# Kernel optimization log

Measured on AMD Instinct MI355X. Metric: run time of the kernel, lower is better.

## Reference

```python
import jax, jax.numpy as jnp
import numpy as np

BN_EPS = 1e-3  # O-CNN default bn_eps


def setup_inputs() -> dict:
    key = jax.random.key(0)
    k1, k2, k3 = jax.random.split(key, 3)
    N, Cin, Cout, K = 100000, 32, 32, 27  # nodes, channels, 3x3x3 taps
    data_in = jax.random.normal(k1, (1, Cin, N, 1), dtype=jnp.float32)
    neigh = jax.random.randint(k2, (N, K), 0, N, dtype=jnp.int32)
    weight = jax.random.normal(k3, (K, Cin, Cout), dtype=jnp.float32) * 0.05
    gamma = jnp.ones((Cout,), dtype=jnp.float32)
    beta = jnp.zeros((Cout,), dtype=jnp.float32)
    return {"data_in": data_in, "neigh": neigh, "weight": weight,
            "gamma": gamma, "beta": beta}


def reference(data_in, neigh, weight, gamma, beta):
    # data_in: [1, Cin, N, 1] -> x: [N, Cin]
    x = data_in[0, :, :, 0].T
    # Octree conv: gather 27 neighbor features per node, then small matmul.
    col = x[neigh]                                   # [N, 27, Cin] (irregular gather)
    y = jnp.einsum('nkc,kcd->nd', col, weight)       # [N, Cout]
    # BatchNorm2d in training mode: stats over the N (spatial) axis.
    mean = jnp.mean(y, axis=0)
    var = jnp.mean(jnp.square(y - mean), axis=0)     # biased variance, as BN uses
    yn = (y - mean) * jax.lax.rsqrt(var + BN_EPS) * gamma + beta
    # back to O-CNN layout [1, Cout, N, 1]
    return yn.T[None, :, :, None]
```

## Files before the change

### kernel.cpp

```cpp
#include <hip/hip_runtime.h>

#define KK 27

typedef short bf16x8 __attribute__((ext_vector_type(8)));
typedef float f32x4  __attribute__((ext_vector_type(4)));

__device__ inline unsigned short f2bf(float f) {
    unsigned u = __float_as_uint(f);
    unsigned r = u + 0x7fffu + ((u >> 16) & 1u);
    return (unsigned short)(r >> 16);
}

__global__ __launch_bounds__(256) void prep_k(const float* __restrict__ in,
                                              const float* __restrict__ w,
                                              unsigned short* __restrict__ xTb,
                                              unsigned short* __restrict__ wTb,
                                              float* __restrict__ tot,
                                              int N, int nxblk) {
    __shared__ float tile[32][33];
    const int b = blockIdx.x;
    if (b < nxblk) {
        int n0 = b * 32;
        int tx = threadIdx.x & 31;
        int ty = threadIdx.x >> 5;
#pragma unroll
        for (int c = ty; c < 32; c += 8) {
            int n = n0 + tx;
            tile[c][tx] = (n < N) ? in[(long)c * N + n] : 0.f;
        }
        __syncthreads();
#pragma unroll
        for (int nn = ty; nn < 32; nn += 8) {
            int n = n0 + nn;
            if (n < N) xTb[(long)n * 32 + tx] = f2bf(tile[tx][nn]);
        }
        if (b == 0 && threadIdx.x < 32) xTb[(long)N * 32 + threadIdx.x] = 0;
    } else {
        int k = b - nxblk;
        for (int i = threadIdx.x; i < 1024; i += 256) {
            int cin = i >> 5, cout = i & 31;
            wTb[k * 1024 + cout * 32 + cin] = f2bf(w[k * 1024 + cin * 32 + cout]);
        }
        if (k == 0) {
            for (int i = threadIdx.x; i < 32 * 64; i += 256) tot[i] = 0.f;
        }
    }
}

__global__ __launch_bounds__(256, 4) void conv_k(const unsigned short* __restrict__ xTb,
                                                 const int* __restrict__ neigh,
                                                 const unsigned short* __restrict__ wTb,
                                                 float* __restrict__ y,
                                                 float* __restrict__ tot,
                                                 int N) {
    __shared__ float ct[4][32][33];

    const int tid  = threadIdx.x;
    const int L    = tid & 63;
    const int w    = tid >> 6;
    const int r16  = L & 15;
    const int quad = L >> 4;
    const int base = blockIdx.x * 128 + w * 32;
    const int n0 = base + r16;
    const int n1 = base + 16 + r16;
    const bool v0 = (n0 < N), v1 = (n1 < N);
    const long nb0 = (long)(v0 ? n0 : 0) * KK;
    const long nb1 = (long)(v1 ? n1 : 0) * KK;

    f32x4 acc00 = {0.f, 0.f, 0.f, 0.f};
    f32x4 acc01 = acc00, acc10 = acc00, acc11 = acc00;

    int ia = v0 ? neigh[nb0] : N;
    int ib = v1 ? neigh[nb1] : N;
    int ja = v0 ? neigh[nb0 + 1] : N;
    int jb = v1 ? neigh[nb1 + 1] : N;

    bf16x8 a0 = *(const bf16x8*)(xTb + (long)ia * 32 + quad * 8);
    bf16x8 a1 = *(const bf16x8*)(xTb + (long)ib * 32 + quad * 8);
    bf16x8 b0 = *(const bf16x8*)(wTb + r16 * 32 + quad * 8);
    bf16x8 b1 = *(const bf16x8*)(wTb + (16 + r16) * 32 + quad * 8);

#pragma unroll 1
    for (int k = 0; k < KK; ++k) {
        bf16x8 na0, na1, pb0, pb1;
        if (k < KK - 1) {
            na0 = *(const bf16x8*)(xTb + (long)ja * 32 + quad * 8);
            na1 = *(const bf16x8*)(xTb + (long)jb * 32 + quad * 8);
            const unsigned short* wn = wTb + (k + 1) * 1024;
            pb0 = *(const bf16x8*)(wn + r16 * 32 + quad * 8);
            pb1 = *(const bf16x8*)(wn + (16 + r16) * 32 + quad * 8);
            int kk = (k + 2 < KK) ? (k + 2) : (KK - 1);
            ja = v0 ? neigh[nb0 + kk] : N;
            jb = v1 ? neigh[nb1 + kk] : N;
        }

        acc00 = __builtin_amdgcn_mfma_f32_16x16x32_bf16(a0, b0, acc00, 0, 0, 0);
        acc01 = __builtin_amdgcn_mfma_f32_16x16x32_bf16(a0, b1, acc01, 0, 0, 0);
        acc10 = __builtin_amdgcn_mfma_f32_16x16x32_bf16(a1, b0, acc10, 0, 0, 0);
        acc11 = __builtin_amdgcn_mfma_f32_16x16x32_bf16(a1, b1, acc11, 0, 0, 0);

        if (k < KK - 1) {
            a0 = na0;
            a1 = na1;
            b0 = pb0;
            b1 = pb1;
        }
    }

    float s0 = 0.f, q0 = 0.f, s1 = 0.f, q1 = 0.f;
#pragma unroll
    for (int r = 0; r < 4; ++r) {
        s0 += acc00[r] + acc10[r];
        q0 += acc00[r] * acc00[r] + acc10[r] * acc10[r];
        s1 += acc01[r] + acc11[r];
        q1 += acc01[r] * acc01[r] + acc11[r] * acc11[r];
    }
#pragma unroll
    for (int off = 16; off < 64; off <<= 1) {
        s0 += __shfl_xor(s0, off, 64);
        q0 += __shfl_xor(q0, off, 64);
        s1 += __shfl_xor(s1, off, 64);
        q1 += __shfl_xor(q1, off, 64);
    }
    const int stripe = (blockIdx.x * 4 + w) & 31;
    if (L < 16) {
        float* tb = tot + stripe * 64;
        atomicAdd(&tb[L],      s0);
        atomicAdd(&tb[L + 16], s1);
        atomicAdd(&tb[L + 32], q0);
        atomicAdd(&tb[L + 48], q1);
    }

#pragma unroll
    for (int r = 0; r < 4; ++r) {
        ct[w][quad * 4 + r][r16]           = acc00[r];
        ct[w][quad * 4 + r][16 + r16]      = acc01[r];
        ct[w][16 + quad * 4 + r][r16]      = acc10[r];
        ct[w][16 + quad * 4 + r][16 + r16] = acc11[r];
    }
    const int node = L & 31;
    const int half = L >> 5;
    const int gn = base + node;
    if (gn < N) {
#pragma unroll
        for (int i = 0; i < 16; ++i) {
            const int cout = i * 2 + half;
            y[(long)cout * N + gn] = ct[w][node][cout];
        }
    }
}

__global__ __launch_bounds__(256) void norm_k(float* __restrict__ y,
                                              const float* __restrict__ tot,
                                              const float* __restrict__ gamma,
                                              const float* __restrict__ beta, int N) {
    const int d = blockIdx.y;
    float sm = 0.f, sq = 0.f;
#pragma unroll
    for (int s = 0; s < 32; ++s) {
        sm += tot[s * 64 + d];
        sq += tot[s * 64 + 32 + d];
    }
    const float mean = sm / (float)N;
    const float var  = sq / (float)N - mean * mean;
    const float sc   = gamma[d] * rsqrtf(var + 1e-3f);
    const float sh   = beta[d] - mean * sc;

    int i = blockIdx.x * blockDim.x + threadIdx.x;
    int base = i * 4;
    if (base + 3 < N) {
        float4* p = (float4*)(y + (long)d * N + base);
        float4 v = *p;
        v.x = fmaf(v.x, sc, sh);
        v.y = fmaf(v.y, sc, sh);
        v.z = fmaf(v.z, sc, sh);
        v.w = fmaf(v.w, sc, sh);
        *p = v;
    } else if (base < N) {
        for (int t = base; t < N; ++t) y[(long)d * N + t] = fmaf(y[(long)d * N + t], sc, sh);
    }
}

extern "C" void kernel_launch(void* const* d_in, const int* in_sizes, int n_in,
                              void* d_out, int out_size, void* d_ws, size_t ws_size,
                              hipStream_t stream) {
    const float* data_in = (const float*)d_in[0];
    const int*   neigh   = (const int*)d_in[1];
    const float* weight  = (const float*)d_in[2];
    const float* gamma   = (const float*)d_in[3];
    const float* beta    = (const float*)d_in[4];
    float* out = (float*)d_out;

    const int N = in_sizes[1] / KK;
    const int nxblk   = (N + 31) / 32;
    const int nblk128 = (N + 127) / 128;

    char* ws = (char*)d_ws;
    unsigned short* xTb = (unsigned short*)ws;
    unsigned short* wTb = (unsigned short*)(ws + (size_t)(N + 1) * 64);
    float* tot = (float*)(ws + (size_t)(N + 1) * 64 + 55296);

    prep_k<<<nxblk + KK, 256, 0, stream>>>(data_in, weight, xTb, wTb, tot, N, nxblk);
    conv_k<<<nblk128, 256, 0, stream>>>(xTb, neigh, wTb, out, tot, N);
    dim3 ngrid(((N + 3) / 4 + 255) / 256, 32);
    norm_k<<<ngrid, 256, 0, stream>>>(out, tot, gamma, beta, N);
}
```

Before: 146.8 us.

## Split bf16 features into channel halves and pair taps per MFMA

Measured after the change: 153.1 us. +4.3%, slower.

```diff
diff --git a/kernel.cpp b/kernel.cpp
--- a/kernel.cpp
+++ b/kernel.cpp
@@ -1,6 +1,8 @@
 #include <hip/hip_runtime.h>
 
+
 #define KK 27
+#define PT 14
 
 typedef short bf16x8 __attribute__((ext_vector_type(8)));
 typedef float f32x4  __attribute__((ext_vector_type(4)));
@@ -13,8 +15,10 @@
 
 __global__ __launch_bounds__(256) void prep_k(const float* __restrict__ in,
                                               const float* __restrict__ w,
-                                              unsigned short* __restrict__ xTb,
-                                              unsigned short* __restrict__ wTb,
+                                              unsigned short* __restrict__ xLo,
+                                              unsigned short* __restrict__ xHi,
+                                              unsigned short* __restrict__ wP0,
+                                              unsigned short* __restrict__ wP1,
                                               float* __restrict__ tot,
                                               int N, int nxblk) {
     __shared__ float tile[32][33];
@@ -32,35 +36,53 @@
 #pragma unroll
         for (int nn = ty; nn < 32; nn += 8) {
             int n = n0 + nn;
-            if (n < N) xTb[(long)n * 32 + tx] = f2bf(tile[tx][nn]);
-        }
-        if (b == 0 && threadIdx.x < 32) xTb[(long)N * 32 + threadIdx.x] = 0;
+            if (n < N) {
+                unsigned short v = f2bf(tile[tx][nn]);
+                if (tx < 16) xLo[(long)n * 16 + tx]        = v;
+                else         xHi[(long)n * 16 + (tx - 16)] = v;
+            }
+        }
+        if (b == 0 && threadIdx.x < 32) {
+            int t = threadIdx.x;
+            if (t < 16) xLo[(long)N * 16 + t]        = 0;
+            else        xHi[(long)N * 16 + (t - 16)] = 0;
+        }
     } else {
-        int k = b - nxblk;
+        int t = b - nxblk;
         for (int i = threadIdx.x; i < 1024; i += 256) {
-            int cin = i >> 5, cout = i & 31;
-            wTb[k * 1024 + cout * 32 + cin] = f2bf(w[k * 1024 + cin * 32 + cout]);
-        }
-        if (k == 0) {
+            int cout = i >> 5, k32 = i & 31;
+            int tap = 2 * t + (k32 >> 4);
+            int c   = k32 & 15;
+            unsigned short lo = 0, hi = 0;
+            if (tap < KK) {
+                lo = f2bf(w[tap * 1024 + c * 32 + cout]);
+                hi = f2bf(w[tap * 1024 + (c + 16) * 32 + cout]);
+            }
+            wP0[t * 1024 + cout * 32 + k32] = lo;
+            wP1[t * 1024 + cout * 32 + k32] = hi;
+        }
+        if (t == 0) {
             for (int i = threadIdx.x; i < 32 * 64; i += 256) tot[i] = 0.f;
         }
     }
 }
 
-__global__ __launch_bounds__(256, 4) void conv_k(const unsigned short* __restrict__ xTb,
-                                                 const int* __restrict__ neigh,
-                                                 const unsigned short* __restrict__ wTb,
-                                                 float* __restrict__ y,
-                                                 float* __restrict__ tot,
-                                                 int N) {
-    __shared__ float ct[4][32][33];
-
-    const int tid  = threadIdx.x;
-    const int L    = tid & 63;
-    const int w    = tid >> 6;
+__global__ __launch_bounds__(64, 4) void conv_k(const unsigned short* __restrict__ xLo,
+                                                const unsigned short* __restrict__ xHi,
+                                                const int* __restrict__ neigh,
+                                                const unsigned short* __restrict__ wP0,
+                                                const unsigned short* __restrict__ wP1,
+                                                float* __restrict__ y,
+                                                float* __restrict__ tot,
+                                                int N) {
+    __shared__ float ct[32][33];
+
+    const int L    = threadIdx.x;
     const int r16  = L & 15;
     const int quad = L >> 4;
-    const int base = blockIdx.x * 128 + w * 32;
+    const int tapsel = quad >> 1;
+    const int off8   = (quad & 1) * 8;
+    const int base = blockIdx.x * 32;
     const int n0 = base + r16;
     const int n1 = base + 16 + r16;
     const bool v0 = (n0 < N), v1 = (n1 < N);
@@ -70,40 +92,51 @@
     f32x4 acc00 = {0.f, 0.f, 0.f, 0.f};
     f32x4 acc01 = acc00, acc10 = acc00, acc11 = acc00;
 
-    int ia = v0 ? neigh[nb0] : N;
-    int ib = v1 ? neigh[nb1] : N;
-    int ja = v0 ? neigh[nb0 + 1] : N;
-    int jb = v1 ? neigh[nb1 + 1] : N;
-
-    bf16x8 a0 = *(const bf16x8*)(xTb + (long)ia * 32 + quad * 8);
-    bf16x8 a1 = *(const bf16x8*)(xTb + (long)ib * 32 + quad * 8);
-    bf16x8 b0 = *(const bf16x8*)(wTb + r16 * 32 + quad * 8);
-    bf16x8 b1 = *(const bf16x8*)(wTb + (16 + r16) * 32 + quad * 8);
+    auto ldidx = [&](long nb, bool v, int kq) -> int {
+        int kc = (kq < KK) ? kq : (KK - 1);
+        int j  = __builtin_nontemporal_load(neigh + nb + kc);
+        return (v && kq < KK) ? j : N;
+    };
 
 #pragma unroll 1
-    for (int k = 0; k < KK; ++k) {
-        bf16x8 na0, na1, pb0, pb1;
-        if (k < KK - 1) {
-            na0 = *(const bf16x8*)(xTb + (long)ja * 32 + quad * 8);
-            na1 = *(const bf16x8*)(xTb + (long)jb * 32 + quad * 8);
-            const unsigned short* wn = wTb + (k + 1) * 1024;
-            pb0 = *(const bf16x8*)(wn + r16 * 32 + quad * 8);
-            pb1 = *(const bf16x8*)(wn + (16 + r16) * 32 + quad * 8);
-            int kk = (k + 2 < KK) ? (k + 2) : (KK - 1);
-            ja = v0 ? neigh[nb0 + kk] : N;
-            jb = v1 ? neigh[nb1 + kk] : N;
-        }
-
-        acc00 = __builtin_amdgcn_mfma_f32_16x16x32_bf16(a0, b0, acc00, 0, 0, 0);
-        acc01 = __builtin_amdgcn_mfma_f32_16x16x32_bf16(a0, b1, acc01, 0, 0, 0);
-        acc10 = __builtin_amdgcn_mfma_f32_16x16x32_bf16(a1, b0, acc10, 0, 0, 0);
-        acc11 = __builtin_amdgcn_mfma_f32_16x16x32_bf16(a1, b1, acc11, 0, 0, 0);
-
-        if (k < KK - 1) {
-            a0 = na0;
-            a1 = na1;
-            b0 = pb0;
-            b1 = pb1;
+    for (int ph = 0; ph < 2; ++ph) {
+        const unsigned short* __restrict__ xp = ph ? xHi : xLo;
+        const unsigned short* __restrict__ wp = ph ? wP1 : wP0;
+
+        int ia = ldidx(nb0, v0, tapsel);
+        int ib = ldidx(nb1, v1, tapsel);
+        int ja = ldidx(nb0, v0, 2 + tapsel);
+        int jb = ldidx(nb1, v1, 2 + tapsel);
+
+        bf16x8 a0 = *(const bf16x8*)(xp + (long)ia * 16 + off8);
+        bf16x8 a1 = *(const bf16x8*)(xp + (long)ib * 16 + off8);
+        bf16x8 b0 = *(const bf16x8*)(wp + r16 * 32 + quad * 8);
+        bf16x8 b1 = *(const bf16x8*)(wp + (16 + r16) * 32 + quad * 8);
+
+#pragma unroll 1
+        for (int t = 0; t < PT; ++t) {
+            bf16x8 na0, na1, pb0, pb1;
+            if (t < PT - 1) {
+                na0 = *(const bf16x8*)(xp + (long)ja * 16 + off8);
+                na1 = *(const bf16x8*)(xp + (long)jb * 16 + off8);
+                const unsigned short* wn = wp + (t + 1) * 1024;
+                pb0 = *(const bf16x8*)(wn + r16 * 32 + quad * 8);
+                pb1 = *(const bf16x8*)(wn + (16 + r16) * 32 + quad * 8);
+                ja = ldidx(nb0, v0, 2 * (t + 2) + tapsel);
+                jb = ldidx(nb1, v1, 2 * (t + 2) + tapsel);
+            }
+
+            acc00 = __builtin_amdgcn_mfma_f32_16x16x32_bf16(a0, b0, acc00, 0, 0, 0);
+            acc01 = __builtin_amdgcn_mfma_f32_16x16x32_bf16(a0, b1, acc01, 0, 0, 0);
+            acc10 = __builtin_amdgcn_mfma_f32_16x16x32_bf16(a1, b0, acc10, 0, 0, 0);
+            acc11 = __builtin_amdgcn_mfma_f32_16x16x32_bf16(a1, b1, acc11, 0, 0, 0);
+
+            if (t < PT - 1) {
+                a0 = na0;
+                a1 = na1;
+                b0 = pb0;
+                b1 = pb1;
+            }
         }
     }
 
@@ -122,7 +155,7 @@
         s1 += __shfl_xor(s1, off, 64);
         q1 += __shfl_xor(q1, off, 64);
     }
-    const int stripe = (blockIdx.x * 4 + w) & 31;
+    const int stripe = blockIdx.x & 31;
     if (L < 16) {
         float* tb = tot + stripe * 64;
         atomicAdd(&tb[L],      s0);
@@ -133,11 +166,12 @@
 
 #pragma unroll
     for (int r = 0; r < 4; ++r) {
-        ct[w][quad * 4 + r][r16]           = acc00[r];
-        ct[w][quad * 4 + r][16 + r16]      = acc01[r];
-        ct[w][16 + quad * 4 + r][r16]      = acc10[r];
-        ct[w][16 + quad * 4 + r][16 + r16] = acc11[r];
-    }
+        ct[quad * 4 + r][r16]           = acc00[r];
+        ct[quad * 4 + r][16 + r16]      = acc01[r];
+        ct[16 + quad * 4 + r][r16]      = acc10[r];
+        ct[16 + quad * 4 + r][16 + r16] = acc11[r];
+    }
+    __syncthreads();
     const int node = L & 31;
     const int half = L >> 5;
     const int gn = base + node;
@@ -145,7 +179,7 @@
 #pragma unroll
         for (int i = 0; i < 16; ++i) {
             const int cout = i * 2 + half;
-            y[(long)cout * N + gn] = ct[w][node][cout];
+            __builtin_nontemporal_store(ct[node][cout], y + (long)cout * N + gn);
         }
     }
 }
@@ -192,16 +226,19 @@
     float* out = (float*)d_out;
 
     const int N = in_sizes[1] / KK;
-    const int nxblk   = (N + 31) / 32;
-    const int nblk128 = (N + 127) / 128;
+    const int nxblk = (N + 31) / 32;
+    const int nblk  = (N + 31) / 32;
 
     char* ws = (char*)d_ws;
-    unsigned short* xTb = (unsigned short*)ws;
-    unsigned short* wTb = (unsigned short*)(ws + (size_t)(N + 1) * 64);
-    float* tot = (float*)(ws + (size_t)(N + 1) * 64 + 55296);
-
-    prep_k<<<nxblk + KK, 256, 0, stream>>>(data_in, weight, xTb, wTb, tot, N, nxblk);
-    conv_k<<<nblk128, 256, 0, stream>>>(xTb, neigh, wTb, out, tot, N);
+    size_t halfBytes = (size_t)(N + 1) * 32;
+    unsigned short* xLo = (unsigned short*)ws;
+    unsigned short* xHi = (unsigned short*)(ws + halfBytes);
+    unsigned short* wP0 = (unsigned short*)(ws + 2 * halfBytes);
+    unsigned short* wP1 = wP0 + PT * 1024;
+    float* tot = (float*)((char*)(wP1 + PT * 1024));
+
+    prep_k<<<nxblk + PT, 256, 0, stream>>>(data_in, weight, xLo, xHi, wP0, wP1, tot, N, nxblk);
+    conv_k<<<nblk, 64, 0, stream>>>(xLo, xHi, neigh, wP0, wP1, out, tot, N);
     dim3 ngrid(((N + 3) / 4 + 255) / 256, 32);
     norm_k<<<ngrid, 256, 0, stream>>>(out, tot, gamma, beta, N);
 }
```

## Split tap loop into two interleaved streams and use one-wave blocks

Applied to the files above, without the earlier changes.

Measured after the change: 135.7 us. -7.5%, faster.

```diff
diff --git a/kernel.cpp b/kernel.cpp
--- a/kernel.cpp
+++ b/kernel.cpp
@@ -47,20 +47,18 @@
     }
 }
 
-__global__ __launch_bounds__(256, 4) void conv_k(const unsigned short* __restrict__ xTb,
-                                                 const int* __restrict__ neigh,
-                                                 const unsigned short* __restrict__ wTb,
-                                                 float* __restrict__ y,
-                                                 float* __restrict__ tot,
-                                                 int N) {
-    __shared__ float ct[4][32][33];
-
-    const int tid  = threadIdx.x;
-    const int L    = tid & 63;
-    const int w    = tid >> 6;
+__global__ __launch_bounds__(64, 4) void conv_k(const unsigned short* __restrict__ xTb,
+                                                const int* __restrict__ neigh,
+                                                const unsigned short* __restrict__ wTb,
+                                                float* __restrict__ y,
+                                                float* __restrict__ tot,
+                                                int N) {
+    __shared__ float ct[32][33];
+
+    const int L    = threadIdx.x;
     const int r16  = L & 15;
     const int quad = L >> 4;
-    const int base = blockIdx.x * 128 + w * 32;
+    const int base = blockIdx.x * 32;
     const int n0 = base + r16;
     const int n1 = base + 16 + r16;
     const bool v0 = (n0 < N), v1 = (n1 < N);
@@ -70,40 +68,60 @@
     f32x4 acc00 = {0.f, 0.f, 0.f, 0.f};
     f32x4 acc01 = acc00, acc10 = acc00, acc11 = acc00;
 
-    int ia = v0 ? neigh[nb0] : N;
-    int ib = v1 ? neigh[nb1] : N;
-    int ja = v0 ? neigh[nb0 + 1] : N;
-    int jb = v1 ? neigh[nb1 + 1] : N;
-
-    bf16x8 a0 = *(const bf16x8*)(xTb + (long)ia * 32 + quad * 8);
-    bf16x8 a1 = *(const bf16x8*)(xTb + (long)ib * 32 + quad * 8);
-    bf16x8 b0 = *(const bf16x8*)(wTb + r16 * 32 + quad * 8);
-    bf16x8 b1 = *(const bf16x8*)(wTb + (16 + r16) * 32 + quad * 8);
+    int iA0 = v0 ? neigh[nb0 + 0]  : N;
+    int iA1 = v1 ? neigh[nb1 + 0]  : N;
+    int iB0 = v0 ? neigh[nb0 + 14] : N;
+    int iB1 = v1 ? neigh[nb1 + 14] : N;
+
+    bf16x8 xA0 = *(const bf16x8*)(xTb + (long)iA0 * 32 + quad * 8);
+    bf16x8 xA1 = *(const bf16x8*)(xTb + (long)iA1 * 32 + quad * 8);
+    bf16x8 xB0 = *(const bf16x8*)(xTb + (long)iB0 * 32 + quad * 8);
+    bf16x8 xB1 = *(const bf16x8*)(xTb + (long)iB1 * 32 + quad * 8);
+
+    bf16x8 wA0 = *(const bf16x8*)(wTb + r16 * 32 + quad * 8);
+    bf16x8 wA1 = *(const bf16x8*)(wTb + (16 + r16) * 32 + quad * 8);
+    bf16x8 wB0 = *(const bf16x8*)(wTb + 14 * 1024 + r16 * 32 + quad * 8);
+    bf16x8 wB1 = *(const bf16x8*)(wTb + 14 * 1024 + (16 + r16) * 32 + quad * 8);
+
+    iA0 = v0 ? neigh[nb0 + 1]  : N;
+    iA1 = v1 ? neigh[nb1 + 1]  : N;
+    iB0 = v0 ? neigh[nb0 + 15] : N;
+    iB1 = v1 ? neigh[nb1 + 15] : N;
 
 #pragma unroll 1
-    for (int k = 0; k < KK; ++k) {
-        bf16x8 na0, na1, pb0, pb1;
-        if (k < KK - 1) {
-            na0 = *(const bf16x8*)(xTb + (long)ja * 32 + quad * 8);
-            na1 = *(const bf16x8*)(xTb + (long)jb * 32 + quad * 8);
-            const unsigned short* wn = wTb + (k + 1) * 1024;
-            pb0 = *(const bf16x8*)(wn + r16 * 32 + quad * 8);
-            pb1 = *(const bf16x8*)(wn + (16 + r16) * 32 + quad * 8);
-            int kk = (k + 2 < KK) ? (k + 2) : (KK - 1);
-            ja = v0 ? neigh[nb0 + kk] : N;
-            jb = v1 ? neigh[nb1 + kk] : N;
-        }
-
-        acc00 = __builtin_amdgcn_mfma_f32_16x16x32_bf16(a0, b0, acc00, 0, 0, 0);
-        acc01 = __builtin_amdgcn_mfma_f32_16x16x32_bf16(a0, b1, acc01, 0, 0, 0);
-        acc10 = __builtin_amdgcn_mfma_f32_16x16x32_bf16(a1, b0, acc10, 0, 0, 0);
-        acc11 = __builtin_amdgcn_mfma_f32_16x16x32_bf16(a1, b1, acc11, 0, 0, 0);
-
-        if (k < KK - 1) {
-            a0 = na0;
-            a1 = na1;
-            b0 = pb0;
-            b1 = pb1;
+    for (int i = 0; i < 14; ++i) {
+        bf16x8 nxA0, nxA1, nxB0, nxB1, nwA0, nwA1, nwB0, nwB1;
+        if (i < 13) {
+            nxA0 = *(const bf16x8*)(xTb + (long)iA0 * 32 + quad * 8);
+            nxA1 = *(const bf16x8*)(xTb + (long)iA1 * 32 + quad * 8);
+            nxB0 = *(const bf16x8*)(xTb + (long)iB0 * 32 + quad * 8);
+            nxB1 = *(const bf16x8*)(xTb + (long)iB1 * 32 + quad * 8);
+            const unsigned short* wa = wTb + (i + 1) * 1024;
+            const int kb = (15 + i <= 26) ? (15 + i) : 26;
+            const unsigned short* wb = wTb + kb * 1024;
+            nwA0 = *(const bf16x8*)(wa + r16 * 32 + quad * 8);
+            nwA1 = *(const bf16x8*)(wa + (16 + r16) * 32 + quad * 8);
+            nwB0 = *(const bf16x8*)(wb + r16 * 32 + quad * 8);
+            nwB1 = *(const bf16x8*)(wb + (16 + r16) * 32 + quad * 8);
+            const int ka2 = (i + 2 <= 13) ? (i + 2) : 13;
+            const int kb2 = (16 + i <= 26) ? (16 + i) : 26;
+            iA0 = v0 ? neigh[nb0 + ka2] : N;
+            iA1 = v1 ? neigh[nb1 + ka2] : N;
+            iB0 = v0 ? neigh[nb0 + kb2] : N;
+            iB1 = v1 ? neigh[nb1 + kb2] : N;
+        }
+
+        acc00 = __builtin_amdgcn_mfma_f32_16x16x32_bf16(xA0, wA0, acc00, 0, 0, 0);
+        acc01 = __builtin_amdgcn_mfma_f32_16x16x32_bf16(xA0, wA1, acc01, 0, 0, 0);
+        acc10 = __builtin_amdgcn_mfma_f32_16x16x32_bf16(xA1, wA0, acc10, 0, 0, 0);
+        acc11 = __builtin_amdgcn_mfma_f32_16x16x32_bf16(xA1, wA1, acc11, 0, 0, 0);
+        if (i < 13) {
+            acc00 = __builtin_amdgcn_mfma_f32_16x16x32_bf16(xB0, wB0, acc00, 0, 0, 0);
+            acc01 = __builtin_amdgcn_mfma_f32_16x16x32_bf16(xB0, wB1, acc01, 0, 0, 0);
+            acc10 = __builtin_amdgcn_mfma_f32_16x16x32_bf16(xB1, wB0, acc10, 0, 0, 0);
+            acc11 = __builtin_amdgcn_mfma_f32_16x16x32_bf16(xB1, wB1, acc11, 0, 0, 0);
+            xA0 = nxA0; xA1 = nxA1; xB0 = nxB0; xB1 = nxB1;
+            wA0 = nwA0; wA1 = nwA1; wB0 = nwB0; wB1 = nwB1;
         }
     }
 
@@ -122,7 +140,7 @@
         s1 += __shfl_xor(s1, off, 64);
         q1 += __shfl_xor(q1, off, 64);
     }
-    const int stripe = (blockIdx.x * 4 + w) & 31;
+    const int stripe = blockIdx.x & 31;
     if (L < 16) {
         float* tb = tot + stripe * 64;
         atomicAdd(&tb[L],      s0);
@@ -133,11 +151,12 @@
 
 #pragma unroll
     for (int r = 0; r < 4; ++r) {
-        ct[w][quad * 4 + r][r16]           = acc00[r];
-        ct[w][quad * 4 + r][16 + r16]      = acc01[r];
-        ct[w][16 + quad * 4 + r][r16]      = acc10[r];
-        ct[w][16 + quad * 4 + r][16 + r16] = acc11[r];
-    }
+        ct[quad * 4 + r][r16]           = acc00[r];
+        ct[quad * 4 + r][16 + r16]      = acc01[r];
+        ct[16 + quad * 4 + r][r16]      = acc10[r];
+        ct[16 + quad * 4 + r][16 + r16] = acc11[r];
+    }
+    __syncthreads();
     const int node = L & 31;
     const int half = L >> 5;
     const int gn = base + node;
@@ -145,7 +164,7 @@
 #pragma unroll
         for (int i = 0; i < 16; ++i) {
             const int cout = i * 2 + half;
-            y[(long)cout * N + gn] = ct[w][node][cout];
+            y[(long)cout * N + gn] = ct[node][cout];
         }
     }
 }
@@ -192,8 +211,8 @@
     float* out = (float*)d_out;
 
     const int N = in_sizes[1] / KK;
-    const int nxblk   = (N + 31) / 32;
-    const int nblk128 = (N + 127) / 128;
+    const int nxblk = (N + 31) / 32;
+    const int nblk  = (N + 31) / 32;
 
     char* ws = (char*)d_ws;
     unsigned short* xTb = (unsigned short*)ws;
@@ -201,7 +220,7 @@
     float* tot = (float*)(ws + (size_t)(N + 1) * 64 + 55296);
 
     prep_k<<<nxblk + KK, 256, 0, stream>>>(data_in, weight, xTb, wTb, tot, N, nxblk);
-    conv_k<<<nblk128, 256, 0, stream>>>(xTb, neigh, wTb, out, tot, N);
+    conv_k<<<nblk, 64, 0, stream>>>(xTb, neigh, wTb, out, tot, N);
     dim3 ngrid(((N + 3) / 4 + 255) / 256, 32);
     norm_k<<<ngrid, 256, 0, stream>>>(out, tot, gamma, beta, N);
 }
```

## Transpose neighbor table to tap-major and use one-wave conv blocks

Applied to the files above, without the earlier changes.

Result: faster. 133.4 us (-9.1%).

```diff
diff --git a/kernel.cpp b/kernel.cpp
--- a/kernel.cpp
+++ b/kernel.cpp
@@ -13,11 +13,14 @@
 
 __global__ __launch_bounds__(256) void prep_k(const float* __restrict__ in,
                                               const float* __restrict__ w,
+                                              const int* __restrict__ neigh,
                                               unsigned short* __restrict__ xTb,
                                               unsigned short* __restrict__ wTb,
+                                              int* __restrict__ neighT,
                                               float* __restrict__ tot,
-                                              int N, int nxblk) {
+                                              int N, int nxblk, int doT) {
     __shared__ float tile[32][33];
+    __shared__ int   nt[64 * KK];
     const int b = blockIdx.x;
     if (b < nxblk) {
         int n0 = b * 32;
@@ -35,7 +38,7 @@
             if (n < N) xTb[(long)n * 32 + tx] = f2bf(tile[tx][nn]);
         }
         if (b == 0 && threadIdx.x < 32) xTb[(long)N * 32 + threadIdx.x] = 0;
-    } else {
+    } else if (b < nxblk + KK) {
         int k = b - nxblk;
         for (int i = threadIdx.x; i < 1024; i += 256) {
             int cin = i >> 5, cout = i & 31;
@@ -44,36 +47,57 @@
         if (k == 0) {
             for (int i = threadIdx.x; i < 32 * 64; i += 256) tot[i] = 0.f;
         }
-    }
-}
-
-__global__ __launch_bounds__(256, 4) void conv_k(const unsigned short* __restrict__ xTb,
-                                                 const int* __restrict__ neigh,
-                                                 const unsigned short* __restrict__ wTb,
-                                                 float* __restrict__ y,
-                                                 float* __restrict__ tot,
-                                                 int N) {
-    __shared__ float ct[4][32][33];
-
-    const int tid  = threadIdx.x;
-    const int L    = tid & 63;
-    const int w    = tid >> 6;
+    } else if (doT) {
+        int t = b - nxblk - KK;
+        int n0 = t * 64;
+        int cnt = N - n0; if (cnt > 64) cnt = 64;
+        for (int i = threadIdx.x; i < cnt * KK; i += 256)
+            nt[i] = neigh[(long)n0 * KK + i];
+        __syncthreads();
+        for (int i = threadIdx.x; i < KK * 64; i += 256) {
+            int tap = i >> 6, n = i & 63;
+            if (n < cnt) neighT[(long)tap * N + n0 + n] = nt[n * KK + tap];
+        }
+    }
+}
+
+template <bool TR>
+__global__ __launch_bounds__(64, 4) void conv_k(const unsigned short* __restrict__ xTb,
+                                                const int* __restrict__ ng,
+                                                const unsigned short* __restrict__ wTb,
+                                                float* __restrict__ y,
+                                                float* __restrict__ tot,
+                                                int N) {
+    __shared__ float ct[32][33];
+
+    const int L    = threadIdx.x;
     const int r16  = L & 15;
     const int quad = L >> 4;
-    const int base = blockIdx.x * 128 + w * 32;
+    const int base = blockIdx.x * 32;
     const int n0 = base + r16;
     const int n1 = base + 16 + r16;
     const bool v0 = (n0 < N), v1 = (n1 < N);
-    const long nb0 = (long)(v0 ? n0 : 0) * KK;
-    const long nb1 = (long)(v1 ? n1 : 0) * KK;
+    const int  n0c = v0 ? n0 : 0;
+    const int  n1c = v1 ? n1 : 0;
+    const long nb0 = (long)n0c * KK;
+    const long nb1 = (long)n1c * KK;
+
+    auto IDX0 = [&](int k) -> int {
+        int j = TR ? ng[(long)k * N + n0c] : ng[nb0 + k];
+        return v0 ? j : N;
+    };
+    auto IDX1 = [&](int k) -> int {
+        int j = TR ? ng[(long)k * N + n1c] : ng[nb1 + k];
+        return v1 ? j : N;
+    };
 
     f32x4 acc00 = {0.f, 0.f, 0.f, 0.f};
     f32x4 acc01 = acc00, acc10 = acc00, acc11 = acc00;
 
-    int ia = v0 ? neigh[nb0] : N;
-    int ib = v1 ? neigh[nb1] : N;
-    int ja = v0 ? neigh[nb0 + 1] : N;
-    int jb = v1 ? neigh[nb1 + 1] : N;
+    int ia = IDX0(0);
+    int ib = IDX1(0);
+    int ja = IDX0(1);
+    int jb = IDX1(1);
 
     bf16x8 a0 = *(const bf16x8*)(xTb + (long)ia * 32 + quad * 8);
     bf16x8 a1 = *(const bf16x8*)(xTb + (long)ib * 32 + quad * 8);
@@ -90,8 +114,8 @@
             pb0 = *(const bf16x8*)(wn + r16 * 32 + quad * 8);
             pb1 = *(const bf16x8*)(wn + (16 + r16) * 32 + quad * 8);
             int kk = (k + 2 < KK) ? (k + 2) : (KK - 1);
-            ja = v0 ? neigh[nb0 + kk] : N;
-            jb = v1 ? neigh[nb1 + kk] : N;
+            ja = IDX0(kk);
+            jb = IDX1(kk);
         }
 
         acc00 = __builtin_amdgcn_mfma_f32_16x16x32_bf16(a0, b0, acc00, 0, 0, 0);
@@ -122,7 +146,7 @@
         s1 += __shfl_xor(s1, off, 64);
         q1 += __shfl_xor(q1, off, 64);
     }
-    const int stripe = (blockIdx.x * 4 + w) & 31;
+    const int stripe = blockIdx.x & 31;
     if (L < 16) {
         float* tb = tot + stripe * 64;
         atomicAdd(&tb[L],      s0);
@@ -133,11 +157,12 @@
 
 #pragma unroll
     for (int r = 0; r < 4; ++r) {
-        ct[w][quad * 4 + r][r16]           = acc00[r];
-        ct[w][quad * 4 + r][16 + r16]      = acc01[r];
-        ct[w][16 + quad * 4 + r][r16]      = acc10[r];
-        ct[w][16 + quad * 4 + r][16 + r16] = acc11[r];
-    }
+        ct[quad * 4 + r][r16]           = acc00[r];
+        ct[quad * 4 + r][16 + r16]      = acc01[r];
+        ct[16 + quad * 4 + r][r16]      = acc10[r];
+        ct[16 + quad * 4 + r][16 + r16] = acc11[r];
+    }
+    __syncthreads();
     const int node = L & 31;
     const int half = L >> 5;
     const int gn = base + node;
@@ -145,7 +170,7 @@
 #pragma unroll
         for (int i = 0; i < 16; ++i) {
             const int cout = i * 2 + half;
-            y[(long)cout * N + gn] = ct[w][node][cout];
+            y[(long)cout * N + gn] = ct[node][cout];
         }
     }
 }
@@ -192,16 +217,26 @@
     float* out = (float*)d_out;
 
     const int N = in_sizes[1] / KK;
-    const int nxblk   = (N + 31) / 32;
-    const int nblk128 = (N + 127) / 128;
+    const int nxblk = (N + 31) / 32;
+    const int nblk  = (N + 31) / 32;
+    const int ntblk = (N + 63) / 64;
 
     char* ws = (char*)d_ws;
     unsigned short* xTb = (unsigned short*)ws;
     unsigned short* wTb = (unsigned short*)(ws + (size_t)(N + 1) * 64);
     float* tot = (float*)(ws + (size_t)(N + 1) * 64 + 55296);
-
-    prep_k<<<nxblk + KK, 256, 0, stream>>>(data_in, weight, xTb, wTb, tot, N, nxblk);
-    conv_k<<<nblk128, 256, 0, stream>>>(xTb, neigh, wTb, out, tot, N);
+    int* neighT = (int*)(ws + (size_t)(N + 1) * 64 + 55296 + 32 * 64 * 4);
+
+    const size_t need = (size_t)(N + 1) * 64 + 55296 + 32 * 64 * 4
+                      + (size_t)KK * N * 4;
+    const int doT = (ws_size >= need) ? 1 : 0;
+
+    prep_k<<<nxblk + KK + (doT ? ntblk : 0), 256, 0, stream>>>(
+        data_in, weight, neigh, xTb, wTb, neighT, tot, N, nxblk, doT);
+    if (doT)
+        conv_k<true><<<nblk, 64, 0, stream>>>(xTb, neighT, wTb, out, tot, N);
+    else
+        conv_k<false><<<nblk, 64, 0, stream>>>(xTb, neigh, wTb, out, tot, N);
     dim3 ngrid(((N + 3) / 4 + 255) / 256, 32);
     norm_k<<<ngrid, 256, 0, stream>>>(out, tot, gamma, beta, N);
 }
```
